# Kernel optimization log

Hardware: AMD Instinct MI355X
Metric: run time of the kernel (lower is better)

The kernel has to match this reference:

```python
import jax, jax.numpy as jnp
import numpy as np
from jax import lax

B, S, D = 1, 512, 2048
HK, HV, DK, DV, K = 8, 16, 128, 128, 4
R = HV // HK
KEY_DIM = HK * DK
VAL_DIM = HV * DV
CONV_DIM = 2 * KEY_DIM + VAL_DIM
EPS = 1e-6


def setup_inputs() -> dict:
    key = jax.random.key(0)
    ks = jax.random.split(key, 8)
    hidden_states = jax.random.normal(ks[0], (B, S, D), jnp.float32)
    W_qkvz = jax.random.normal(ks[1], (D, 2 * KEY_DIM + 2 * VAL_DIM), jnp.float32) * 0.02
    W_ba = jax.random.normal(ks[2], (D, 2 * HV), jnp.float32) * 0.02
    conv_w = jax.random.normal(ks[3], (CONV_DIM, 1, K), jnp.float32) * 0.2  # depthwise [C,1,K]
    dt_bias = jnp.ones((HV,), jnp.float32)
    A_log = jnp.log(jax.random.uniform(ks[4], (HV,), jnp.float32, 1e-3, 16.0))
    norm_weight = jnp.ones((DV,), jnp.float32)
    W_out = jax.random.normal(ks[5], (VAL_DIM, D), jnp.float32) * 0.02
    return dict(hidden_states=hidden_states, W_qkvz=W_qkvz, W_ba=W_ba, conv_w=conv_w,
                dt_bias=dt_bias, A_log=A_log, norm_weight=norm_weight, W_out=W_out)


def _l2norm(x):
    return x * lax.rsqrt(jnp.sum(x * x, -1, keepdims=True) + EPS)


def reference(hidden_states, W_qkvz, W_ba, conv_w, dt_bias, A_log, norm_weight, W_out):
    # input projections
    qkvz = hidden_states @ W_qkvz              # [B,S,2*key_dim+2*value_dim]
    ba = hidden_states @ W_ba                  # [B,S,2*HV]
    # _rearrange: split per key-head group
    qkvz = qkvz.reshape(B, S, HK, 2 * DK + 2 * R * DV)
    q = qkvz[..., :DK]                                         # [B,S,HK,DK]
    k = qkvz[..., DK:2 * DK]                                   # [B,S,HK,DK]
    v = qkvz[..., 2 * DK:2 * DK + R * DV].reshape(B, S, HV, DV)
    z = qkvz[..., 2 * DK + R * DV:].reshape(B, S, HV, DV)
    ba = ba.reshape(B, S, HK, 2 * R)
    b = ba[..., :R].reshape(B, S, HV)
    a = ba[..., R:].reshape(B, S, HV)
    # fused causal depthwise conv1d + SiLU over concat(q,k,v)
    mixed = jnp.concatenate([q.reshape(B, S, -1), k.reshape(B, S, -1), v.reshape(B, S, -1)], -1)
    mixed = mixed.transpose(0, 2, 1)           # [B,C,S]
    mixed = lax.conv_general_dilated(mixed, conv_w, (1,), [(K - 1, 0)],
                                     feature_group_count=CONV_DIM,
                                     dimension_numbers=('NCH', 'OIH', 'NCH'))
    mixed = jax.nn.silu(mixed).transpose(0, 2, 1)  # [B,S,C]
    q = mixed[..., :KEY_DIM].reshape(B, S, HK, DK)
    k = mixed[..., KEY_DIM:2 * KEY_DIM].reshape(B, S, HK, DK)
    v = mixed[..., 2 * KEY_DIM:].reshape(B, S, HV, DV)
    # gates
    beta = jax.nn.sigmoid(b)                                   # [B,S,HV]
    g = jnp.exp(-jnp.exp(A_log) * jax.nn.softplus(a + dt_bias))  # per-step decay in (0,1)
    q = _l2norm(q) * (DK ** -0.5)
    k = _l2norm(k)
    q = jnp.repeat(q, R, axis=2)               # GQA expand to HV heads
    k = jnp.repeat(k, R, axis=2)
    # gated delta-rule recurrence over sequence (state per batch/head: [DK,DV])
    def step(Sst, inp):
        qt, kt, vt, gt, bt = inp
        Sst = Sst * gt[..., None, None]
        pred = jnp.einsum('bhk,bhkv->bhv', kt, Sst)
        delta = (vt - pred) * bt[..., None]
        Sst = Sst + jnp.einsum('bhk,bhv->bhkv', kt, delta)
        o = jnp.einsum('bhk,bhkv->bhv', qt, Sst)
        return Sst, o
    xs = (q.transpose(1, 0, 2, 3), k.transpose(1, 0, 2, 3), v.transpose(1, 0, 2, 3),
          g.transpose(1, 0, 2), beta.transpose(1, 0, 2))
    S0 = jnp.zeros((B, HV, DK, DV), jnp.float32)
    _, core = lax.scan(step, S0, xs)           # core: [S,B,HV,DV]
    core = core.transpose(1, 0, 2, 3)          # [B,S,HV,DV]
    # gated RMSNorm per value head, gated by silu(z)
    var = jnp.mean(core * core, -1, keepdims=True)
    normed = core * lax.rsqrt(var + EPS) * norm_weight * jax.nn.silu(z)
    return normed.reshape(B, S, VAL_DIM) @ W_out
```

## Files before the change

### kernel.cpp

```cpp
#include <hip/hip_runtime.h>
#include <hip/hip_bf16.h>
#include <math.h>

#define S_  512
#define D_  2048
#define HK_ 8
#define HV_ 16
#define DK_ 128
#define DV_ 128
#define KEY_DIM_ 1024
#define VAL_DIM_ 2048
#define QKVZ_N  6144
#define EPS_ 1e-6f

typedef __attribute__((ext_vector_type(8))) short short8;
typedef __attribute__((ext_vector_type(4))) float f32x4;
typedef __attribute__((ext_vector_type(2))) float v2f;
typedef unsigned short ushort_t;
typedef unsigned int uint_t;

__device__ __forceinline__ ushort_t f2bf(float x) {
    uint_t u = __float_as_uint(x);
    return (ushort_t)((u + 0x7FFFu + ((u >> 16) & 1u)) >> 16);
}

__device__ __forceinline__ void gl2lds16(const void* g, void* l) {
    __builtin_amdgcn_global_load_lds((const __attribute__((address_space(1))) uint_t*)g,
                                     (__attribute__((address_space(3))) uint_t*)l, 16, 0, 0);
}
__device__ __forceinline__ void gl2lds4(const void* g, void* l) {
    __builtin_amdgcn_global_load_lds((const __attribute__((address_space(1))) uint_t*)g,
                                     (__attribute__((address_space(3))) uint_t*)l, 4, 0, 0);
}

__global__ __launch_bounds__(256) void convert_bf16(const float* __restrict__ X,
                                                    ushort_t* __restrict__ H, int n4) {
    int i = blockIdx.x * blockDim.x + threadIdx.x;
    if (i >= n4) return;
    float4 v = ((const float4*)X)[i];
    ushort4 h;
    h.x = f2bf(v.x); h.y = f2bf(v.y); h.z = f2bf(v.z); h.w = f2bf(v.w);
    ((ushort4*)H)[i] = h;
}

__global__ __launch_bounds__(256) void transpose_convert(const float* __restrict__ W,
                                                         ushort_t* __restrict__ Th,
                                                         int K, int N) {
    __shared__ float tile[64][65];
    const int kb = blockIdx.y * 64, nb = blockIdx.x * 64;
    const int t = threadIdx.x;
#pragma unroll
    for (int i = 0; i < 4; ++i) {
        int r = (t >> 4) + i * 16;
        int c4 = (t & 15) * 4;
        float4 v = *(const float4*)&W[(size_t)(kb + r) * N + nb + c4];
        tile[r][c4 + 0] = v.x; tile[r][c4 + 1] = v.y;
        tile[r][c4 + 2] = v.z; tile[r][c4 + 3] = v.w;
    }
    __syncthreads();
#pragma unroll
    for (int i = 0; i < 4; ++i) {
        int idx = t + 256 * i;
        int n = idx >> 4;
        int k4 = (idx & 15) * 4;
        ushort4 h;
        h.x = f2bf(tile[k4 + 0][n]); h.y = f2bf(tile[k4 + 1][n]);
        h.z = f2bf(tile[k4 + 2][n]); h.w = f2bf(tile[k4 + 3][n]);
        *(ushort4*)&Th[(size_t)(nb + n) * K + kb + k4] = h;
    }
}

template<int BM, int BN, int WR, int WC>
__global__ __launch_bounds__(256) void gemm_bf16(const ushort_t* __restrict__ A,
                                                 const ushort_t* __restrict__ B,
                                                 float* __restrict__ C,
                                                 int M, int N, int K) {
    constexpr int TM = BM / (16 * WR);
    constexpr int TN = BN / (16 * WC);
    constexpr int AI = (BM / 16) * 2;
    constexpr int BI = (BN / 16) * 2;

    __shared__ __align__(16) ushort_t sA[2][2][BM][32];
    __shared__ __align__(16) ushort_t sB[2][2][BN][32];

    const int t = threadIdx.x;
    const int w = t >> 6, lane = t & 63;
    const int wr = w / WC, wc = w % WC;
    const int lm = lane & 15, quad = lane >> 4;
    const int m0 = blockIdx.y * BM, n0 = blockIdx.x * BN;
    const int lrow = lane >> 2;
    const int lch  = (lane & 3) * 8;

    auto stage = [&](int buf, int k0) {
#pragma unroll
        for (int j = w; j < AI; j += 4) {
            int ks = j & 1, r0 = (j >> 1) * 16;
            gl2lds16(&A[(size_t)(m0 + r0 + lrow) * K + k0 + ks * 32 + lch],
                     &sA[buf][ks][r0][0]);
        }
#pragma unroll
        for (int j = w; j < BI; j += 4) {
            int ks = j & 1, r0 = (j >> 1) * 16;
            gl2lds16(&B[(size_t)(n0 + r0 + lrow) * K + k0 + ks * 32 + lch],
                     &sB[buf][ks][r0][0]);
        }
    };

    f32x4 acc[TM][TN] = {};
    stage(0, 0);
    __syncthreads();

    const int NK = K / 64;
    for (int it = 0; it < NK; ++it) {
        int buf = it & 1;
        if (it + 1 < NK) stage(buf ^ 1, (it + 1) * 64);
#pragma unroll
        for (int ks = 0; ks < 2; ++ks) {
            short8 bf[TN];
#pragma unroll
            for (int ni = 0; ni < TN; ++ni)
                bf[ni] = *(const short8*)&sB[buf][ks][wc * (TN * 16) + ni * 16 + lm][quad * 8];
#pragma unroll
            for (int mi = 0; mi < TM; ++mi) {
                short8 af = *(const short8*)&sA[buf][ks][wr * (TM * 16) + mi * 16 + lm][quad * 8];
#pragma unroll
                for (int ni = 0; ni < TN; ++ni)
                    acc[mi][ni] = __builtin_amdgcn_mfma_f32_16x16x32_bf16(af, bf[ni], acc[mi][ni], 0, 0, 0);
            }
        }
        __syncthreads();
    }

#pragma unroll
    for (int mi = 0; mi < TM; ++mi)
#pragma unroll
        for (int ni = 0; ni < TN; ++ni) {
            int row = m0 + wr * TM * 16 + mi * 16 + quad * 4;
            int col = n0 + wc * TN * 16 + ni * 16 + lm;
#pragma unroll
            for (int r = 0; r < 4; ++r)
                C[(size_t)(row + r) * N + col] = acc[mi][ni][r];
        }
}

__global__ __launch_bounds__(256) void ba_kernel(const float* __restrict__ hid,
                                                 const float* __restrict__ Wba,
                                                 float* __restrict__ ba) {
    const int s = blockIdx.x;
    const int j = threadIdx.x & 31;
    const int kg = threadIdx.x >> 5;
    const float* h = hid + (size_t)s * D_;
    float sum = 0.f;
    const int k0 = kg * 256;
#pragma unroll 8
    for (int k = k0; k < k0 + 256; ++k)
        sum = fmaf(h[k], Wba[(size_t)k * 32 + j], sum);
    __shared__ float red[8][32];
    red[kg][j] = sum;
    __syncthreads();
    if (threadIdx.x < 32) {
        float tot = 0.f;
#pragma unroll
        for (int r = 0; r < 8; ++r) tot += red[r][j];
        ba[s * 32 + j] = tot;
    }
}

__global__ __launch_bounds__(128) void conv_kernel(const float* __restrict__ qkvz,
                                                   const float* __restrict__ conv_w,
                                                   float* __restrict__ qc,
                                                   float* __restrict__ kc,
                                                   float* __restrict__ vc) {
    const int s   = blockIdx.x;
    const int grp = blockIdx.y;
    const int d   = threadIdx.x;

    int col, c;
    if (grp < 8) {
        int hk = grp;
        col = hk * 768 + d;
        c   = hk * 128 + d;
    } else if (grp < 16) {
        int hk = grp - 8;
        col = hk * 768 + 128 + d;
        c   = 1024 + (hk * 128 + d);
    } else {
        int hv = grp - 16;
        col = (hv >> 1) * 768 + 256 + (hv & 1) * 128 + d;
        c   = 2048 + (hv * 128 + d);
    }

    const float w0 = conv_w[c * 4 + 0];
    const float w1 = conv_w[c * 4 + 1];
    const float w2 = conv_w[c * 4 + 2];
    const float w3 = conv_w[c * 4 + 3];

    float x = 0.f;
    if (s - 3 >= 0) x += qkvz[(size_t)(s - 3) * QKVZ_N + col] * w0;
    if (s - 2 >= 0) x += qkvz[(size_t)(s - 2) * QKVZ_N + col] * w1;
    if (s - 1 >= 0) x += qkvz[(size_t)(s - 1) * QKVZ_N + col] * w2;
    x += qkvz[(size_t)s * QKVZ_N + col] * w3;

    x = x / (1.f + expf(-x));

    if (grp < 16) {
        float ss = x * x;
#pragma unroll
        for (int m = 1; m < 64; m <<= 1) ss += __shfl_xor(ss, m);
        __shared__ float red[2];
        int wid = threadIdx.x >> 6;
        if ((threadIdx.x & 63) == 0) red[wid] = ss;
        __syncthreads();
        float tot = red[0] + red[1];
        float scale = rsqrtf(tot + EPS_);
        if (grp < 8) {
            x = x * scale * 0.08838834764831845f;
            qc[((size_t)s * HK_ + grp) * DK_ + d] = x;
        } else {
            x = x * scale;
            kc[((size_t)s * HK_ + (grp - 8)) * DK_ + d] = x;
        }
    } else {
        vc[((size_t)s * HV_ + (grp - 16)) * DV_ + d] = x;
    }
}

template<int CTRL>
__device__ __forceinline__ float dpp_xor(float x) {
    int v = __builtin_amdgcn_update_dpp(0, __float_as_int(x), CTRL, 0xF, 0xF, true);
    return __int_as_float(v);
}
__device__ __forceinline__ float red16(float x) {
    x += dpp_xor<0xB1>(x);
    x += dpp_xor<0x4E>(x);
    x += dpp_xor<0x141>(x);
    x += dpp_xor<0x140>(x);
    return x;
}
__device__ __forceinline__ float red32(float x) {
    x = red16(x);
    x += __int_as_float(__builtin_amdgcn_ds_swizzle(__float_as_int(x), 0x401F));
    return x;
}

__device__ __forceinline__ float gate_g(float a, float Aexp) {
    float sp = (a > 20.f) ? a : log1pf(expf(a));
    return expf(-Aexp * sp);
}

__global__ __launch_bounds__(256) void scal_kernel(const float* __restrict__ kc,
                                                   const float* __restrict__ ba,
                                                   const float* __restrict__ A_log,
                                                   const float* __restrict__ dt_bias,
                                                   float* __restrict__ scal) {
    const int t  = blockIdx.x;
    const int hk = threadIdx.x >> 5;
    const int s32 = threadIdx.x & 31;

    float c = 0.f;
    if (t > 0) {
        float4 kt = *(const float4*)&kc[((size_t)t * HK_ + hk) * DK_ + s32 * 4];
        float4 kp = *(const float4*)&kc[((size_t)(t - 1) * HK_ + hk) * DK_ + s32 * 4];
        c = kt.x * kp.x + kt.y * kp.y + kt.z * kp.z + kt.w * kp.w;
    }
    c = red32(c);

    if (s32 < 2) {
        int r = s32;
        int h = hk * 2 + r;
        float Aexp = expf(A_log[h]);
        float dtb  = dt_bias[h];
        float bv = ba[t * 32 + hk * 4 + r];
        float av = ba[t * 32 + hk * 4 + 2 + r];
        float bt = 1.f / (1.f + expf(-bv));
        float gt = gate_g(av + dtb, Aexp);
        float gp = 0.f;
        if (t > 0) {
            float ap = ba[(t - 1) * 32 + hk * 4 + 2 + r];
            gp = gate_g(ap + dtb, Aexp);
        }
        float4 o;
        o.x = -gt * c * bt;
        o.y = gt * gp;
        o.z = bt;
        o.w = gt;
        *(float4*)&scal[((size_t)h * S_ + t) * 4] = o;
    }
}

__global__ __launch_bounds__(64) void scan_kernel(const float* __restrict__ qc,
                                                  const float* __restrict__ kc,
                                                  const float* __restrict__ vc,
                                                  const float* __restrict__ scal,
                                                  float* __restrict__ core) {
    const int h = blockIdx.y, v0 = blockIdx.x * 8;
    const int lane = threadIdx.x;
    const int sub = lane & 15, colg = lane >> 4;
    const int hk = h >> 1;

    __shared__ __align__(16) float skq[2][32][256];
    __shared__ __align__(16) float sv[2][32][8];
    __shared__ __align__(16) float ssc[2][32][4];

    auto stage = [&](int buf, int c) {
        const int t0 = c * 32;
        for (int j = 0; j < 32; ++j) {
            int tt = t0 + j;
            const float* src = (lane < 32)
                ? &kc[((size_t)tt * HK_ + hk) * DK_ + lane * 4]
                : &qc[((size_t)tt * HK_ + hk) * DK_ + (lane - 32) * 4];
            gl2lds16(src, &skq[buf][j][0]);
        }
#pragma unroll
        for (int i = 0; i < 4; ++i) {
            int tt = t0 + i * 8 + (lane >> 3);
            gl2lds4(&vc[((size_t)tt * HV_ + h) * DV_ + v0 + (lane & 7)],
                    &sv[buf][i * 8][0]);
        }
#pragma unroll
        for (int i = 0; i < 2; ++i)
            gl2lds4(&scal[((size_t)h * S_ + t0) * 4 + i * 64 + lane],
                    ((float*)&ssc[buf][0][0]) + i * 64);
    };

    v2f  S0[4] = {}, S1[4] = {};
    v2f  kS[4][4] = {}, qS[4][4] = {};
    float vS[4][2] = {};
    float4 scS[4] = {};
    float D0 = 0.f, D1 = 0.f;

    stage(0, 0);
    __syncthreads();

    auto rd = [&](int slot, int buf, int j) {
#pragma unroll
        for (int i = 0; i < 4; ++i) {
            kS[slot][i] = *(const v2f*)&skq[buf][j][sub * 8 + i * 2];
            qS[slot][i] = *(const v2f*)&skq[buf][j][128 + sub * 8 + i * 2];
        }
        vS[slot][0] = sv[buf][j][colg];
        vS[slot][1] = sv[buf][j][colg + 4];
        scS[slot] = *(const float4*)&ssc[buf][j][0];
    };

    rd(0, 0, 0);
    rd(1, 0, 1);

    for (int c = 0; c < 16; ++c) {
        const int buf = c & 1;
        if (c + 1 < 16) stage(buf ^ 1, c + 1);

#pragma unroll
        for (int j = 0; j < 32; ++j) {
            const int cur = j & 3, prv = (j + 3) & 3;
            if (j < 30) rd((j + 2) & 3, buf, j + 2);

            v2f ua = kS[cur][0] * S0[0] + kS[cur][1] * S0[1]
                   + kS[cur][2] * S0[2] + kS[cur][3] * S0[3];
            v2f ub = kS[cur][0] * S1[0] + kS[cur][1] * S1[1]
                   + kS[cur][2] * S1[2] + kS[cur][3] * S1[3];
            float Ua = red16(ua.x + ua.y);
            float Ub = red16(ub.x + ub.y);

            const float gp = scS[prv].w;
            const v2f gp2 = {gp, gp};
            const v2f Da2 = {D0, D0}, Db2 = {D1, D1};
#pragma unroll
            for (int i = 0; i < 4; ++i) {
                S0[i] = kS[prv][i] * Da2 + gp2 * S0[i];
                S1[i] = kS[prv][i] * Db2 + gp2 * S1[i];
            }

            v2f oa = qS[prv][0] * S0[0] + qS[prv][1] * S0[1]
                   + qS[prv][2] * S0[2] + qS[prv][3] * S0[3];
            v2f ob = qS[prv][0] * S1[0] + qS[prv][1] * S1[1]
                   + qS[prv][2] * S1[2] + qS[prv][3] * S1[3];
            float Oa = red16(oa.x + oa.y);
            float Ob = red16(ob.x + ob.y);
            const int tg = c * 32 + j;
            if (sub == 0 && tg > 0) {
                core[((size_t)(tg - 1) * HV_ + h) * DV_ + v0 + colg] = Oa;
                core[((size_t)(tg - 1) * HV_ + h) * DV_ + v0 + colg + 4] = Ob;
            }

            const float P = scS[cur].x, W1 = scS[cur].y, be = scS[cur].z;
            D0 = fmaf(P, D0, (vS[cur][0] - W1 * Ua) * be);
            D1 = fmaf(P, D1, (vS[cur][1] - W1 * Ub) * be);
        }
        __syncthreads();
        if (c + 1 < 16) {
            rd(0, buf ^ 1, 0);
            rd(1, buf ^ 1, 1);
        }
    }

    {
        const float gp = scS[3].w;
        const v2f gp2 = {gp, gp};
        const v2f Da2 = {D0, D0}, Db2 = {D1, D1};
#pragma unroll
        for (int i = 0; i < 4; ++i) {
            S0[i] = kS[3][i] * Da2 + gp2 * S0[i];
            S1[i] = kS[3][i] * Db2 + gp2 * S1[i];
        }
        v2f oa = qS[3][0] * S0[0] + qS[3][1] * S0[1]
               + qS[3][2] * S0[2] + qS[3][3] * S0[3];
        v2f ob = qS[3][0] * S1[0] + qS[3][1] * S1[1]
               + qS[3][2] * S1[2] + qS[3][3] * S1[3];
        float Oa = red16(oa.x + oa.y);
        float Ob = red16(ob.x + ob.y);
        if (sub == 0) {
            core[((size_t)(S_ - 1) * HV_ + h) * DV_ + v0 + colg] = Oa;
            core[((size_t)(S_ - 1) * HV_ + h) * DV_ + v0 + colg + 4] = Ob;
        }
    }
}

__global__ __launch_bounds__(128) void normgate_kernel(const float* __restrict__ core,
                                                       const float* __restrict__ qkvz,
                                                       const float* __restrict__ nw,
                                                       ushort_t* __restrict__ nh) {
    const int s  = blockIdx.x;
    const int hv = blockIdx.y;
    const int d  = threadIdx.x;

    float x = core[((size_t)s * HV_ + hv) * DV_ + d];
    float ss = x * x;
#pragma unroll
    for (int m = 1; m < 64; m <<= 1) ss += __shfl_xor(ss, m);
    __shared__ float red[2];
    int wid = threadIdx.x >> 6;
    if ((threadIdx.x & 63) == 0) red[wid] = ss;
    __syncthreads();
    float var = (red[0] + red[1]) * (1.f / 128.f);
    float rs  = rsqrtf(var + EPS_);

    float z  = qkvz[(size_t)s * QKVZ_N + (hv >> 1) * 768 + 512 + (hv & 1) * 128 + d];
    float sz = z / (1.f + expf(-z));

    float y = x * rs * nw[d] * sz;
    nh[(size_t)s * VAL_DIM_ + hv * DV_ + d] = f2bf(y);
}

extern "C" void kernel_launch(void* const* d_in, const int* in_sizes, int n_in,
                              void* d_out, int out_size, void* d_ws, size_t ws_size,
                              hipStream_t stream) {
    const float* hidden  = (const float*)d_in[0];
    const float* W_qkvz  = (const float*)d_in[1];
    const float* W_ba    = (const float*)d_in[2];
    const float* conv_w  = (const float*)d_in[3];
    const float* dt_bias = (const float*)d_in[4];
    const float* A_log   = (const float*)d_in[5];
    const float* norm_w  = (const float*)d_in[6];
    const float* W_out   = (const float*)d_in[7];
    float* out = (float*)d_out;

    char* w = (char*)d_ws;
    auto alloc = [&](size_t bytes) { char* p = w; w += (bytes + 255) & ~(size_t)255; return p; };

    float*    qkvz = (float*)alloc((size_t)S_ * QKVZ_N * 4);
    float*    ba   = (float*)alloc((size_t)S_ * 32 * 4);
    float*    qc   = (float*)alloc((size_t)S_ * KEY_DIM_ * 4);
    float*    kc   = (float*)alloc((size_t)S_ * KEY_DIM_ * 4);
    float*    vc   = (float*)alloc((size_t)S_ * VAL_DIM_ * 4);
    float*    scal = (float*)alloc((size_t)HV_ * S_ * 4 * 4);
    float*    core = (float*)alloc((size_t)S_ * VAL_DIM_ * 4);
    ushort_t* hidh = (ushort_t*)alloc((size_t)S_ * D_ * 2);
    ushort_t* nrmh = (ushort_t*)alloc((size_t)S_ * VAL_DIM_ * 2);
    ushort_t* Wqh  = (ushort_t*)alloc((size_t)D_ * QKVZ_N * 2);
    ushort_t* Woh  = (ushort_t*)alloc((size_t)VAL_DIM_ * D_ * 2);

    convert_bf16<<<dim3((S_ * D_ / 4 + 255) / 256), 256, 0, stream>>>(hidden, hidh, S_ * D_ / 4);
    transpose_convert<<<dim3(QKVZ_N / 64, D_ / 64), 256, 0, stream>>>(W_qkvz, Wqh, D_, QKVZ_N);
    transpose_convert<<<dim3(D_ / 64, VAL_DIM_ / 64), 256, 0, stream>>>(W_out, Woh, VAL_DIM_, D_);

    gemm_bf16<64, 128, 1, 4><<<dim3(QKVZ_N / 128, S_ / 64), 256, 0, stream>>>(
        hidh, Wqh, qkvz, S_, QKVZ_N, D_);

    ba_kernel<<<dim3(S_), 256, 0, stream>>>(hidden, W_ba, ba);

    conv_kernel<<<dim3(S_, 32), 128, 0, stream>>>(qkvz, conv_w, qc, kc, vc);

    scal_kernel<<<dim3(S_), 256, 0, stream>>>(kc, ba, A_log, dt_bias, scal);

    scan_kernel<<<dim3(DV_ / 8, HV_), 64, 0, stream>>>(qc, kc, vc, scal, core);

    normgate_kernel<<<dim3(S_, HV_), 128, 0, stream>>>(core, qkvz, norm_w, nrmh);

    gemm_bf16<64, 64, 2, 2><<<dim3(D_ / 64, S_ / 64), 256, 0, stream>>>(
        nrmh, Woh, out, S_, D_, VAL_DIM_);
}
```

Before: 299.1 us.

## Deepen delta-rule scan lookahead to four steps with precomputed coupling scalars

Extends the scalar precompute kernel to produce k-k and q-k dot products and cumulative gate products spanning the previous three timesteps. This lets the scan kernel defer state updates and shorten the serial dependency chain between reductions and delta updates. The scan block now uses two wavefronts with one value column per lane group instead of two per lane. Buffers are padded so the lookahead can read past the sequence end. The price is more scalar precompute, more registers, and extra LDS staging for the head of the next chunk.

```diff
diff --git a/kernel.cpp b/kernel.cpp
--- a/kernel.cpp
+++ b/kernel.cpp
@@ -12,6 +12,7 @@
 #define VAL_DIM_ 2048
 #define QKVZ_N  6144
 #define EPS_ 1e-6f
+#define SPAD_ (S_ + 8)
 
 typedef __attribute__((ext_vector_type(8))) short short8;
 typedef __attribute__((ext_vector_type(4))) float f32x4;
@@ -249,170 +250,203 @@
 }
 
 __global__ __launch_bounds__(256) void scal_kernel(const float* __restrict__ kc,
+                                                   const float* __restrict__ qc,
                                                    const float* __restrict__ ba,
                                                    const float* __restrict__ A_log,
                                                    const float* __restrict__ dt_bias,
                                                    float* __restrict__ scal) {
     const int t  = blockIdx.x;
     const int hk = threadIdx.x >> 5;
-    const int s32 = threadIdx.x & 31;
-
-    float c = 0.f;
-    if (t > 0) {
-        float4 kt = *(const float4*)&kc[((size_t)t * HK_ + hk) * DK_ + s32 * 4];
-        float4 kp = *(const float4*)&kc[((size_t)(t - 1) * HK_ + hk) * DK_ + s32 * 4];
-        c = kt.x * kp.x + kt.y * kp.y + kt.z * kp.z + kt.w * kp.w;
-    }
-    c = red32(c);
-
-    if (s32 < 2) {
-        int r = s32;
-        int h = hk * 2 + r;
+    const int l  = threadIdx.x & 31;
+
+    const float* kt = &kc[((size_t)t * HK_ + hk) * DK_ + l * 4];
+    const float* qt = &qc[((size_t)t * HK_ + hk) * DK_ + l * 4];
+    const float4 zz = {0.f, 0.f, 0.f, 0.f};
+    float4 k0 = *(const float4*)kt;
+    float4 q0 = *(const float4*)qt;
+    float4 k1 = (t >= 1) ? *(const float4*)(kt - (size_t)HK_ * DK_)     : zz;
+    float4 k2 = (t >= 2) ? *(const float4*)(kt - (size_t)2 * HK_ * DK_) : zz;
+    float4 k3 = (t >= 3) ? *(const float4*)(kt - (size_t)3 * HK_ * DK_) : zz;
+
+    auto dot4 = [](float4 a, float4 b) { return a.x*b.x + a.y*b.y + a.z*b.z + a.w*b.w; };
+    float c1 = red32(dot4(k0, k1));
+    float c2 = red32(dot4(k0, k2));
+    float c3 = red32(dot4(k0, k3));
+    float d0 = red32(dot4(q0, k0));
+    float d1 = red32(dot4(q0, k1));
+    float d2 = red32(dot4(q0, k2));
+    float d3 = red32(dot4(q0, k3));
+
+    if (l < 2) {
+        int h = hk * 2 + l;
         float Aexp = expf(A_log[h]);
         float dtb  = dt_bias[h];
-        float bv = ba[t * 32 + hk * 4 + r];
-        float av = ba[t * 32 + hk * 4 + 2 + r];
-        float bt = 1.f / (1.f + expf(-bv));
-        float gt = gate_g(av + dtb, Aexp);
-        float gp = 0.f;
-        if (t > 0) {
-            float ap = ba[(t - 1) * 32 + hk * 4 + 2 + r];
-            gp = gate_g(ap + dtb, Aexp);
-        }
-        float4 o;
-        o.x = -gt * c * bt;
-        o.y = gt * gp;
-        o.z = bt;
-        o.w = gt;
-        *(float4*)&scal[((size_t)h * S_ + t) * 4] = o;
-    }
-}
-
-__global__ __launch_bounds__(64) void scan_kernel(const float* __restrict__ qc,
-                                                  const float* __restrict__ kc,
-                                                  const float* __restrict__ vc,
-                                                  const float* __restrict__ scal,
-                                                  float* __restrict__ core) {
+        float bv = ba[t * 32 + hk * 4 + l];
+        float av = ba[t * 32 + hk * 4 + 2 + l];
+        float be = 1.f / (1.f + expf(-bv));
+        float g0 = gate_g(av + dtb, Aexp);
+        float g1 = 1.f, g2 = 1.f, g3 = 1.f;
+        if (t >= 1) g1 = gate_g(ba[(t - 1) * 32 + hk * 4 + 2 + l] + dtb, Aexp);
+        if (t >= 2) g2 = gate_g(ba[(t - 2) * 32 + hk * 4 + 2 + l] + dtb, Aexp);
+        if (t >= 3) g3 = gate_g(ba[(t - 3) * 32 + hk * 4 + 2 + l] + dtb, Aexp);
+        float G2 = g0 * g1, G3 = G2 * g2, G4 = G3 * g3;
+        float4 oC = {g0, be, G4, 0.f};
+        float4 oA = {-be * g0 * c1, -be * G2 * c2, -be * G3 * c3, -be * G4};
+        float4 oB = {d0, g0 * d1, G2 * d2, G3 * d3};
+        float* dst = &scal[(size_t)(h * SPAD_ + t) * 16];
+        *(float4*)&dst[0]  = oC;
+        *(float4*)&dst[4]  = oA;
+        *(float4*)&dst[8]  = oB;
+        *(float4*)&dst[12] = zz;
+    }
+}
+
+__global__ __launch_bounds__(128) void scan_kernel(const float* __restrict__ qc,
+                                                   const float* __restrict__ kc,
+                                                   const float* __restrict__ vc,
+                                                   const float* __restrict__ scal,
+                                                   float* __restrict__ core) {
     const int h = blockIdx.y, v0 = blockIdx.x * 8;
-    const int lane = threadIdx.x;
+    const int tid = threadIdx.x;
+    const int w = tid >> 6, lane = tid & 63;
     const int sub = lane & 15, colg = lane >> 4;
+    const int vloc = w * 4 + colg;
+    const int v = v0 + vloc;
     const int hk = h >> 1;
 
     __shared__ __align__(16) float skq[2][32][256];
     __shared__ __align__(16) float sv[2][32][8];
-    __shared__ __align__(16) float ssc[2][32][4];
-
-    auto stage = [&](int buf, int c) {
+    __shared__ __align__(16) float ssc[2][32][16];
+    __shared__ __align__(16) float hkq[2][4][256];
+    __shared__ __align__(16) float hv[2][4][8];
+    __shared__ __align__(16) float hsc[2][4][16];
+
+    auto stage_chunk = [&](int buf, int c) {
         const int t0 = c * 32;
-        for (int j = 0; j < 32; ++j) {
+        for (int j = w * 16; j < w * 16 + 16; ++j) {
             int tt = t0 + j;
             const float* src = (lane < 32)
                 ? &kc[((size_t)tt * HK_ + hk) * DK_ + lane * 4]
                 : &qc[((size_t)tt * HK_ + hk) * DK_ + (lane - 32) * 4];
             gl2lds16(src, &skq[buf][j][0]);
         }
+        if (w == 0) {
+#pragma unroll
+            for (int i = 0; i < 4; ++i) {
+                int tt = t0 + i * 8 + (lane >> 3);
+                gl2lds4(&vc[((size_t)tt * HV_ + h) * DV_ + v0 + (lane & 7)],
+                        &sv[buf][i * 8][0]);
+            }
+        } else {
+#pragma unroll
+            for (int i = 0; i < 2; ++i)
+                gl2lds16(&scal[(size_t)(h * SPAD_ + t0) * 16 + i * 256 + lane * 4],
+                         &ssc[buf][i * 16][0]);
+        }
+    };
+    auto stage_head = [&](int c) {
+        const int hb = c & 1;
+        const int t0 = c * 32;
+        if (w == 1) {
+#pragma unroll
+            for (int j = 0; j < 4; ++j) {
+                int tt = t0 + j;
+                const float* src = (lane < 32)
+                    ? &kc[((size_t)tt * HK_ + hk) * DK_ + lane * 4]
+                    : &qc[((size_t)tt * HK_ + hk) * DK_ + (lane - 32) * 4];
+                gl2lds16(src, &hkq[hb][j][0]);
+            }
+        } else {
+            if (lane < 32)
+                gl2lds4(&vc[((size_t)(t0 + (lane >> 3)) * HV_ + h) * DV_ + v0 + (lane & 7)],
+                        &hv[hb][0][0]);
+            if (lane < 16)
+                gl2lds16(&scal[(size_t)(h * SPAD_ + t0) * 16 + lane * 4],
+                         &hsc[hb][0][0]);
+        }
+    };
+
+    v2f Sr[4] = {};
+    v2f kR[8][4] = {};
+    v2f qR[4][4] = {};
+    float vR[4] = {};
+    float4 scA[4] = {}, scB[4] = {}, scC[4] = {};
+    float U[4] = {}, V[4] = {}, dl[4] = {};
+
+    stage_chunk(0, 0);
+    stage_head(1);
+    __syncthreads();
+
+#pragma unroll
+    for (int p = 0; p < 4; ++p)
 #pragma unroll
         for (int i = 0; i < 4; ++i) {
-            int tt = t0 + i * 8 + (lane >> 3);
-            gl2lds4(&vc[((size_t)tt * HV_ + h) * DV_ + v0 + (lane & 7)],
-                    &sv[buf][i * 8][0]);
-        }
-#pragma unroll
-        for (int i = 0; i < 2; ++i)
-            gl2lds4(&scal[((size_t)h * S_ + t0) * 4 + i * 64 + lane],
-                    ((float*)&ssc[buf][0][0]) + i * 64);
-    };
-
-    v2f  S0[4] = {}, S1[4] = {};
-    v2f  kS[4][4] = {}, qS[4][4] = {};
-    float vS[4][2] = {};
-    float4 scS[4] = {};
-    float D0 = 0.f, D1 = 0.f;
-
-    stage(0, 0);
-    __syncthreads();
-
-    auto rd = [&](int slot, int buf, int j) {
-#pragma unroll
-        for (int i = 0; i < 4; ++i) {
-            kS[slot][i] = *(const v2f*)&skq[buf][j][sub * 8 + i * 2];
-            qS[slot][i] = *(const v2f*)&skq[buf][j][128 + sub * 8 + i * 2];
-        }
-        vS[slot][0] = sv[buf][j][colg];
-        vS[slot][1] = sv[buf][j][colg + 4];
-        scS[slot] = *(const float4*)&ssc[buf][j][0];
-    };
-
-    rd(0, 0, 0);
-    rd(1, 0, 1);
+            kR[p][i] = *(const v2f*)&skq[0][p][sub * 8 + i * 2];
+            qR[p][i] = *(const v2f*)&skq[0][p][128 + sub * 8 + i * 2];
+        }
+#pragma unroll
+    for (int p = 0; p < 2; ++p) {
+        scC[p] = *(const float4*)&ssc[0][p][0];
+        scA[p] = *(const float4*)&ssc[0][p][4];
+        scB[p] = *(const float4*)&ssc[0][p][8];
+        vR[p] = sv[0][p][vloc];
+    }
 
     for (int c = 0; c < 16; ++c) {
         const int buf = c & 1;
-        if (c + 1 < 16) stage(buf ^ 1, c + 1);
+        const int hb = (c + 1) & 1;
+        if (c + 1 < 16) stage_chunk(buf ^ 1, c + 1);
+        if (c + 2 < 16) stage_head(c + 2);
+        const int t0 = c * 32;
 
 #pragma unroll
         for (int j = 0; j < 32; ++j) {
-            const int cur = j & 3, prv = (j + 3) & 3;
-            if (j < 30) rd((j + 2) & 3, buf, j + 2);
-
-            v2f ua = kS[cur][0] * S0[0] + kS[cur][1] * S0[1]
-                   + kS[cur][2] * S0[2] + kS[cur][3] * S0[3];
-            v2f ub = kS[cur][0] * S1[0] + kS[cur][1] * S1[1]
-                   + kS[cur][2] * S1[2] + kS[cur][3] * S1[3];
-            float Ua = red16(ua.x + ua.y);
-            float Ub = red16(ub.x + ub.y);
-
-            const float gp = scS[prv].w;
-            const v2f gp2 = {gp, gp};
-            const v2f Da2 = {D0, D0}, Db2 = {D1, D1};
-#pragma unroll
-            for (int i = 0; i < 4; ++i) {
-                S0[i] = kS[prv][i] * Da2 + gp2 * S0[i];
-                S1[i] = kS[prv][i] * Db2 + gp2 * S1[i];
-            }
-
-            v2f oa = qS[prv][0] * S0[0] + qS[prv][1] * S0[1]
-                   + qS[prv][2] * S0[2] + qS[prv][3] * S0[3];
-            v2f ob = qS[prv][0] * S1[0] + qS[prv][1] * S1[1]
-                   + qS[prv][2] * S1[2] + qS[prv][3] * S1[3];
-            float Oa = red16(oa.x + oa.y);
-            float Ob = red16(ob.x + ob.y);
-            const int tg = c * 32 + j;
-            if (sub == 0 && tg > 0) {
-                core[((size_t)(tg - 1) * HV_ + h) * DV_ + v0 + colg] = Oa;
-                core[((size_t)(tg - 1) * HV_ + h) * DV_ + v0 + colg + 4] = Ob;
-            }
-
-            const float P = scS[cur].x, W1 = scS[cur].y, be = scS[cur].z;
-            D0 = fmaf(P, D0, (vS[cur][0] - W1 * Ua) * be);
-            D1 = fmaf(P, D1, (vS[cur][1] - W1 * Ub) * be);
+            {
+                const float g  = ((const float*)&scC[(j + 2) & 3])[0];
+                const float dd = dl[(j + 2) & 3];
+                const v2f g2 = {g, g}, dd2 = {dd, dd};
+#pragma unroll
+                for (int i = 0; i < 4; ++i)
+                    Sr[i] = kR[(j + 6) & 7][i] * dd2 + g2 * Sr[i];
+            }
+            {
+                const float* kb = (j < 28) ? &skq[buf][j + 4][0] : &hkq[hb][j - 28][0];
+#pragma unroll
+                for (int i = 0; i < 4; ++i) {
+                    kR[(j + 4) & 7][i] = *(const v2f*)&kb[sub * 8 + i * 2];
+                    qR[(j + 4) & 3][i] = *(const v2f*)&kb[128 + sub * 8 + i * 2];
+                }
+            }
+            {
+                const float* sb = (j < 30) ? &ssc[buf][j + 2][0] : &hsc[hb][j - 30][0];
+                scC[(j + 2) & 3] = *(const float4*)&sb[0];
+                scA[(j + 2) & 3] = *(const float4*)&sb[4];
+                scB[(j + 2) & 3] = *(const float4*)&sb[8];
+                const float* vb = (j < 30) ? &sv[buf][j + 2][0] : &hv[hb][j - 30][0];
+                vR[(j + 2) & 3] = vb[vloc];
+            }
+            {
+                v2f ua = kR[(j + 2) & 7][0] * Sr[0] + kR[(j + 2) & 7][1] * Sr[1]
+                       + kR[(j + 2) & 7][2] * Sr[2] + kR[(j + 2) & 7][3] * Sr[3];
+                v2f va = qR[(j + 2) & 3][0] * Sr[0] + qR[(j + 2) & 3][1] * Sr[1]
+                       + qR[(j + 2) & 3][2] * Sr[2] + qR[(j + 2) & 3][3] * Sr[3];
+                U[(j + 2) & 3] = red16(ua.x + ua.y);
+                V[(j + 2) & 3] = red16(va.x + va.y);
+            }
+            {
+                const float4 A = scA[j & 3], B = scB[j & 3], Cc = scC[j & 3];
+                const float d1 = dl[(j + 3) & 3], d2 = dl[(j + 2) & 3], d3 = dl[(j + 1) & 3];
+                const float E = fmaf(A.w, U[j & 3], Cc.y * vR[j & 3]);
+                const float X = fmaf(A.y, d2, fmaf(A.z, d3, E));
+                const float dn = fmaf(A.x, d1, X);
+                const float o = fmaf(B.x, dn, fmaf(B.y, d1,
+                                  fmaf(B.z, d2, fmaf(B.w, d3, Cc.z * V[j & 3]))));
+                if (sub == 0)
+                    core[((size_t)(t0 + j) * HV_ + h) * DV_ + v] = o;
+                dl[j & 3] = dn;
+            }
         }
         __syncthreads();
-        if (c + 1 < 16) {
-            rd(0, buf ^ 1, 0);
-            rd(1, buf ^ 1, 1);
-        }
-    }
-
-    {
-        const float gp = scS[3].w;
-        const v2f gp2 = {gp, gp};
-        const v2f Da2 = {D0, D0}, Db2 = {D1, D1};
-#pragma unroll
-        for (int i = 0; i < 4; ++i) {
-            S0[i] = kS[3][i] * Da2 + gp2 * S0[i];
-            S1[i] = kS[3][i] * Db2 + gp2 * S1[i];
-        }
-        v2f oa = qS[3][0] * S0[0] + qS[3][1] * S0[1]
-               + qS[3][2] * S0[2] + qS[3][3] * S0[3];
-        v2f ob = qS[3][0] * S1[0] + qS[3][1] * S1[1]
-               + qS[3][2] * S1[2] + qS[3][3] * S1[3];
-        float Oa = red16(oa.x + oa.y);
-        float Ob = red16(ob.x + ob.y);
-        if (sub == 0) {
-            core[((size_t)(S_ - 1) * HV_ + h) * DV_ + v0 + colg] = Oa;
-            core[((size_t)(S_ - 1) * HV_ + h) * DV_ + v0 + colg + 4] = Ob;
-        }
     }
 }
 
@@ -460,10 +494,10 @@
 
     float*    qkvz = (float*)alloc((size_t)S_ * QKVZ_N * 4);
     float*    ba   = (float*)alloc((size_t)S_ * 32 * 4);
-    float*    qc   = (float*)alloc((size_t)S_ * KEY_DIM_ * 4);
-    float*    kc   = (float*)alloc((size_t)S_ * KEY_DIM_ * 4);
-    float*    vc   = (float*)alloc((size_t)S_ * VAL_DIM_ * 4);
-    float*    scal = (float*)alloc((size_t)HV_ * S_ * 4 * 4);
+    float*    qc   = (float*)alloc((size_t)SPAD_ * KEY_DIM_ * 4);
+    float*    kc   = (float*)alloc((size_t)SPAD_ * KEY_DIM_ * 4);
+    float*    vc   = (float*)alloc((size_t)SPAD_ * VAL_DIM_ * 4);
+    float*    scal = (float*)alloc((size_t)HV_ * SPAD_ * 16 * 4);
     float*    core = (float*)alloc((size_t)S_ * VAL_DIM_ * 4);
     ushort_t* hidh = (ushort_t*)alloc((size_t)S_ * D_ * 2);
     ushort_t* nrmh = (ushort_t*)alloc((size_t)S_ * VAL_DIM_ * 2);
@@ -481,9 +515,9 @@
 
     conv_kernel<<<dim3(S_, 32), 128, 0, stream>>>(qkvz, conv_w, qc, kc, vc);
 
-    scal_kernel<<<dim3(S_), 256, 0, stream>>>(kc, ba, A_log, dt_bias, scal);
-
-    scan_kernel<<<dim3(DV_ / 8, HV_), 64, 0, stream>>>(qc, kc, vc, scal, core);
+    scal_kernel<<<dim3(S_), 256, 0, stream>>>(kc, qc, ba, A_log, dt_bias, scal);
+
+    scan_kernel<<<dim3(DV_ / 8, HV_), 128, 0, stream>>>(qc, kc, vc, scal, core);
 
     normgate_kernel<<<dim3(S_, HV_), 128, 0, stream>>>(core, qkvz, norm_w, nrmh);
 
```

Result: faster. 287.1 us (-4.0%).
